# Kernel optimization log

Hardware: AMD Instinct MI355X
Metric: run time of the kernel (lower is better)

The kernel has to match this reference:

```python
import jax, jax.numpy as jnp
import numpy as np

# init kwargs (constants)
MIN_ = 1      # bg samples
MAX_ = 1      # fg samples
KSZ = 3       # dilation kernel size
IGNORE = -255 # seg_ignore_idx
EPS = 1e-6

B, H, W = 128, 512, 512


def setup_inputs() -> dict:
    key = jax.random.key(0)
    k1, k2, k3 = jax.random.split(key, 3)
    x = jax.random.uniform(k1, (B, 1, H, W), dtype=jnp.float32)   # CAM, nonneg
    u_fg = jax.random.uniform(k2, (B, H * W), dtype=jnp.float32)  # noise for fg multinomial
    u_bg = jax.random.uniform(k3, (B, H * W), dtype=jnp.float32)  # noise for bg multinomial
    return {"x": x, "u_fg": u_fg, "u_bg": u_bg}


def _sample_mask(logw, u, k):
    """Weighted sampling without replacement via Gumbel-top-k (== torch.multinomial).
    logw: [B, HW] log-weights; u: [B, HW] uniform noise. Returns binary [B, HW] int32 mask."""
    g = -jnp.log(-jnp.log(jnp.clip(u, 1e-12, 1.0 - 1e-12)))
    idx = jax.lax.top_k(logw + g, k)[1]  # [B, k]
    mask = jnp.zeros(logw.shape, dtype=jnp.int32)
    return mask.at[jnp.arange(logw.shape[0])[:, None], idx].set(1)


def _dilate(m):
    """Morphological dilation of binary mask [B,H,W] with KSZ x KSZ ones structuring element
    == max-pool with SAME padding."""
    if KSZ == 1:
        return m
    return jax.lax.reduce_window(m, jnp.int32(0), jax.lax.max,
                                 (1, KSZ, KSZ), (1, 1, 1), 'SAME')


def reference(x, u_fg, u_bg):
    b, _, h, w = x.shape
    cam = x[:, 0].reshape(b, h * w)
    p = cam + EPS
    p = p / p.sum(axis=1, keepdims=True)           # normalized CAM (fg weights)
    fg = _sample_mask(jnp.log(p), u_fg, MAX_).reshape(b, h, w)
    bg = _sample_mask(jnp.log1p(-p), u_bg, MIN_).reshape(b, h, w)  # bg weights = 1 - p
    fg = _dilate(fg)
    bg = _dilate(bg)
    overlap = (fg + bg) == 2
    fg = jnp.where(overlap, 0, fg)
    bg = jnp.where(overlap, 0, bg)
    out = jnp.full((b, h, w), IGNORE, dtype=jnp.int32)
    out = jnp.where(fg == 1, 1, out)
    out = jnp.where(bg == 1, 0, out)  # bg written last, as in torch
    return out
```

## Files before the change

### kernel.cpp

```cpp
#include <hip/hip_runtime.h>

#define NB 128
#define HH 512
#define WW 512
#define HW (HH * WW)

constexpr float EPS_F = 1e-6f;
constexpr int IGNORE_V = -255;

constexpr int TPB = 256;
constexpr int G = 4;
constexpr int NG = 4;
constexpr int F4T = G * NG;
constexpr int EPB = TPB * F4T * 4;
constexpr int BPR = HW / EPB;

typedef float floatx4 __attribute__((ext_vector_type(4)));
typedef int intx4 __attribute__((ext_vector_type(4)));

__device__ inline unsigned long long pack_key(float f, unsigned idx) {
    unsigned bits = __float_as_uint(f);
    bits ^= (bits & 0x80000000u) ? 0xFFFFFFFFu : 0x80000000u;
    return ((unsigned long long)bits << 32) | (unsigned)(~idx);
}

__global__ __launch_bounds__(TPB, 4) void k_fg_sum_fill(const float* __restrict__ cam,
                                                        const float* __restrict__ ufg,
                                                        int* __restrict__ out,
                                                        float* __restrict__ partial,
                                                        unsigned long long* __restrict__ bestFg) {
    const int b = blockIdx.y, chunk = blockIdx.x, t = threadIdx.x;
    const long base = (long)b * HW + (long)chunk * EPB;
    const floatx4* c4 = (const floatx4*)(cam + base);
    const floatx4* f4 = (const floatx4*)(ufg + base);
    intx4* o4 = (intx4*)(out + base);
    const intx4 fill = {IGNORE_V, IGNORE_V, IGNORE_V, IGNORE_V};

    floatx4 cb[2][G], ub[2][G];
#pragma unroll
    for (int k = 0; k < G; ++k) {
        cb[0][k] = c4[t + k * TPB];
        ub[0][k] = __builtin_nontemporal_load(&f4[t + k * TPB]);
    }

    float s = 0.f;
    unsigned long long bf = 0ull;
#pragma unroll
    for (int g = 0; g < NG; ++g) {
        const int cur = g & 1, nxt = cur ^ 1;
        if (g + 1 < NG) {
#pragma unroll
            for (int k = 0; k < G; ++k) {
                cb[nxt][k] = c4[t + ((g + 1) * G + k) * TPB];
                ub[nxt][k] = __builtin_nontemporal_load(&f4[t + ((g + 1) * G + k) * TPB]);
            }
        }
#pragma unroll
        for (int k = 0; k < G; ++k) {
            const int slot = g * G + k;
            __builtin_nontemporal_store(fill, &o4[t + slot * TPB]);
            floatx4 v = cb[cur][k];
            floatx4 uu = ub[cur][k];
            const unsigned idx0 = (unsigned)chunk * (unsigned)EPB + (unsigned)(t + slot * TPB) * 4u;
#pragma unroll
            for (int j = 0; j < 4; ++j) {
                float a = v[j] + EPS_F;
                s += a;
                float E = -logf(fmaxf(uu[j], 1e-12f));
                unsigned long long kf = pack_key(a / E, idx0 + j);
                bf = kf > bf ? kf : bf;
            }
        }
    }

#pragma unroll
    for (int off = 32; off > 0; off >>= 1) {
        s += __shfl_down(s, off, 64);
        unsigned long long of = __shfl_down(bf, off, 64);
        bf = of > bf ? of : bf;
    }
    __shared__ float ls[TPB / 64];
    __shared__ unsigned long long lf[TPB / 64];
    if ((t & 63) == 0) { ls[t >> 6] = s; lf[t >> 6] = bf; }
    __syncthreads();
    if (t == 0) {
        float tot = 0.f;
#pragma unroll
        for (int w = 0; w < TPB / 64; ++w) {
            tot += ls[w];
            if (lf[w] > bf) bf = lf[w];
        }
        partial[b * BPR + chunk] = tot;
        bestFg[b * BPR + chunk] = bf;
    }
}

__global__ __launch_bounds__(TPB, 4) void k_bg(const float* __restrict__ cam,
                                               const float* __restrict__ ubg,
                                               const float* __restrict__ partial,
                                               unsigned long long* __restrict__ bestBg) {
    const int b = blockIdx.y, chunk = blockIdx.x, t = threadIdx.x;

    float S = 0.f;
    for (int i = 0; i < BPR; ++i) S += partial[b * BPR + i];

    const long base = (long)b * HW + (long)chunk * EPB;
    const floatx4* c4 = (const floatx4*)(cam + base);
    const floatx4* g4 = (const floatx4*)(ubg + base);

    floatx4 cb[2][G], ub[2][G];
#pragma unroll
    for (int k = 0; k < G; ++k) {
        cb[0][k] = __builtin_nontemporal_load(&c4[t + k * TPB]);
        ub[0][k] = __builtin_nontemporal_load(&g4[t + k * TPB]);
    }

    unsigned long long bb = 0ull;
#pragma unroll
    for (int g = 0; g < NG; ++g) {
        const int cur = g & 1, nxt = cur ^ 1;
        if (g + 1 < NG) {
#pragma unroll
            for (int k = 0; k < G; ++k) {
                cb[nxt][k] = __builtin_nontemporal_load(&c4[t + ((g + 1) * G + k) * TPB]);
                ub[nxt][k] = __builtin_nontemporal_load(&g4[t + ((g + 1) * G + k) * TPB]);
            }
        }
#pragma unroll
        for (int k = 0; k < G; ++k) {
            const int slot = g * G + k;
            floatx4 v = cb[cur][k];
            floatx4 uu = ub[cur][k];
            const unsigned idx0 = (unsigned)chunk * (unsigned)EPB + (unsigned)(t + slot * TPB) * 4u;
#pragma unroll
            for (int j = 0; j < 4; ++j) {
                float num = S - (v[j] + EPS_F);
                float E = -logf(fmaxf(uu[j], 1e-12f));
                unsigned long long kb = pack_key(num / E, idx0 + j);
                bb = kb > bb ? kb : bb;
            }
        }
    }

#pragma unroll
    for (int off = 32; off > 0; off >>= 1) {
        unsigned long long ob = __shfl_down(bb, off, 64);
        bb = ob > bb ? ob : bb;
    }
    __shared__ unsigned long long lb[TPB / 64];
    if ((t & 63) == 0) lb[t >> 6] = bb;
    __syncthreads();
    if (t == 0) {
        for (int w = 1; w < TPB / 64; ++w)
            if (lb[w] > bb) bb = lb[w];
        bestBg[b * BPR + chunk] = bb;
    }
}

__global__ void k_fixup(const unsigned long long* __restrict__ bestFg,
                        const unsigned long long* __restrict__ bestBg,
                        int* __restrict__ out) {
    const int b = threadIdx.x;
    if (b >= NB) return;
    unsigned long long bf = 0ull, bb = 0ull;
    for (int i = 0; i < BPR; ++i) {
        unsigned long long f = bestFg[b * BPR + i];
        unsigned long long g = bestBg[b * BPR + i];
        if (f > bf) bf = f;
        if (g > bb) bb = g;
    }
    const unsigned fidx = ~(unsigned)(bf & 0xFFFFFFFFull);
    const unsigned bidx = ~(unsigned)(bb & 0xFFFFFFFFull);
    const int fr = (int)(fidx / WW), fc = (int)(fidx % WW);
    const int br = (int)(bidx / WW), bc = (int)(bidx % WW);
    const long rb = (long)b * HW;

    for (int dr = -1; dr <= 1; ++dr) {
        for (int dc = -1; dc <= 1; ++dc) {
            int r = fr + dr, c = fc + dc;
            if (r >= 0 && r < HH && c >= 0 && c < WW) {
                bool inBg = (r >= br - 1 && r <= br + 1 && c >= bc - 1 && c <= bc + 1);
                if (!inBg) out[rb + (long)r * WW + c] = 1;
            }
            r = br + dr; c = bc + dc;
            if (r >= 0 && r < HH && c >= 0 && c < WW) {
                bool inFg = (r >= fr - 1 && r <= fr + 1 && c >= fc - 1 && c <= fc + 1);
                if (!inFg) out[rb + (long)r * WW + c] = 0;
            }
        }
    }
}

extern "C" void kernel_launch(void* const* d_in, const int* in_sizes, int n_in,
                              void* d_out, int out_size, void* d_ws, size_t ws_size,
                              hipStream_t stream) {
    const float* cam = (const float*)d_in[0];
    const float* ufg = (const float*)d_in[1];
    const float* ubg = (const float*)d_in[2];
    int* out = (int*)d_out;

    float* partial = (float*)d_ws;
    unsigned long long* bestFg = (unsigned long long*)((char*)d_ws + 8192);
    unsigned long long* bestBg = (unsigned long long*)((char*)d_ws + 24576);

    dim3 grid(BPR, NB);
    k_fg_sum_fill<<<grid, TPB, 0, stream>>>(cam, ufg, out, partial, bestFg);
    k_bg<<<grid, TPB, 0, stream>>>(cam, ubg, partial, bestBg);
    k_fixup<<<1, 128, 0, stream>>>(bestFg, bestBg, out);
}
```

Measured before the change: 412.1 us.

## Move fg scoring into second pass alongside bg scoring

The fg Gumbel-max scoring, along with its read of the u_fg noise, moves out of the first kernel, which now only sums the CAM and fills the output. The second kernel reads cam, u_fg and u_bg together and computes both fg and bg keys, using smaller prefetch groups to keep register pressure in check. Total bytes moved stay about the same. The work between the two passes is rebalanced: the first pass becomes a light streaming pass and the second carries both log-heavy computations. The second kernel now holds more registers per thread and issues more loads in flight.

```diff
diff --git a/kernel.cpp b/kernel.cpp
--- a/kernel.cpp
+++ b/kernel.cpp
@@ -15,6 +15,9 @@
 constexpr int EPB = TPB * F4T * 4;
 constexpr int BPR = HW / EPB;
 
+constexpr int G2 = 2;
+constexpr int NG2 = 8;
+
 typedef float floatx4 __attribute__((ext_vector_type(4)));
 typedef int intx4 __attribute__((ext_vector_type(4)));
 
@@ -24,81 +27,59 @@
     return ((unsigned long long)bits << 32) | (unsigned)(~idx);
 }
 
-__global__ __launch_bounds__(TPB, 4) void k_fg_sum_fill(const float* __restrict__ cam,
-                                                        const float* __restrict__ ufg,
-                                                        int* __restrict__ out,
-                                                        float* __restrict__ partial,
-                                                        unsigned long long* __restrict__ bestFg) {
+__global__ __launch_bounds__(TPB, 4) void k_sum_fill(const float* __restrict__ cam,
+                                                     int* __restrict__ out,
+                                                     float* __restrict__ partial) {
     const int b = blockIdx.y, chunk = blockIdx.x, t = threadIdx.x;
     const long base = (long)b * HW + (long)chunk * EPB;
     const floatx4* c4 = (const floatx4*)(cam + base);
-    const floatx4* f4 = (const floatx4*)(ufg + base);
     intx4* o4 = (intx4*)(out + base);
     const intx4 fill = {IGNORE_V, IGNORE_V, IGNORE_V, IGNORE_V};
 
-    floatx4 cb[2][G], ub[2][G];
-#pragma unroll
-    for (int k = 0; k < G; ++k) {
-        cb[0][k] = c4[t + k * TPB];
-        ub[0][k] = __builtin_nontemporal_load(&f4[t + k * TPB]);
-    }
+    floatx4 cb[2][G];
+#pragma unroll
+    for (int k = 0; k < G; ++k) cb[0][k] = c4[t + k * TPB];
 
     float s = 0.f;
-    unsigned long long bf = 0ull;
 #pragma unroll
     for (int g = 0; g < NG; ++g) {
         const int cur = g & 1, nxt = cur ^ 1;
         if (g + 1 < NG) {
 #pragma unroll
-            for (int k = 0; k < G; ++k) {
-                cb[nxt][k] = c4[t + ((g + 1) * G + k) * TPB];
-                ub[nxt][k] = __builtin_nontemporal_load(&f4[t + ((g + 1) * G + k) * TPB]);
-            }
+            for (int k = 0; k < G; ++k) cb[nxt][k] = c4[t + ((g + 1) * G + k) * TPB];
         }
 #pragma unroll
         for (int k = 0; k < G; ++k) {
             const int slot = g * G + k;
             __builtin_nontemporal_store(fill, &o4[t + slot * TPB]);
             floatx4 v = cb[cur][k];
-            floatx4 uu = ub[cur][k];
-            const unsigned idx0 = (unsigned)chunk * (unsigned)EPB + (unsigned)(t + slot * TPB) * 4u;
 #pragma unroll
             for (int j = 0; j < 4; ++j) {
                 float a = v[j] + EPS_F;
                 s += a;
-                float E = -logf(fmaxf(uu[j], 1e-12f));
-                unsigned long long kf = pack_key(a / E, idx0 + j);
-                bf = kf > bf ? kf : bf;
-            }
-        }
-    }
-
-#pragma unroll
-    for (int off = 32; off > 0; off >>= 1) {
-        s += __shfl_down(s, off, 64);
-        unsigned long long of = __shfl_down(bf, off, 64);
-        bf = of > bf ? of : bf;
-    }
+            }
+        }
+    }
+
+#pragma unroll
+    for (int off = 32; off > 0; off >>= 1) s += __shfl_down(s, off, 64);
     __shared__ float ls[TPB / 64];
-    __shared__ unsigned long long lf[TPB / 64];
-    if ((t & 63) == 0) { ls[t >> 6] = s; lf[t >> 6] = bf; }
+    if ((t & 63) == 0) ls[t >> 6] = s;
     __syncthreads();
     if (t == 0) {
         float tot = 0.f;
 #pragma unroll
-        for (int w = 0; w < TPB / 64; ++w) {
-            tot += ls[w];
-            if (lf[w] > bf) bf = lf[w];
-        }
+        for (int w = 0; w < TPB / 64; ++w) tot += ls[w];
         partial[b * BPR + chunk] = tot;
-        bestFg[b * BPR + chunk] = bf;
-    }
-}
-
-__global__ __launch_bounds__(TPB, 4) void k_bg(const float* __restrict__ cam,
-                                               const float* __restrict__ ubg,
-                                               const float* __restrict__ partial,
-                                               unsigned long long* __restrict__ bestBg) {
+    }
+}
+
+__global__ __launch_bounds__(TPB, 4) void k_score(const float* __restrict__ cam,
+                                                  const float* __restrict__ ufg,
+                                                  const float* __restrict__ ubg,
+                                                  const float* __restrict__ partial,
+                                                  unsigned long long* __restrict__ bestFg,
+                                                  unsigned long long* __restrict__ bestBg) {
     const int b = blockIdx.y, chunk = blockIdx.x, t = threadIdx.x;
 
     float S = 0.f;
@@ -106,37 +87,44 @@
 
     const long base = (long)b * HW + (long)chunk * EPB;
     const floatx4* c4 = (const floatx4*)(cam + base);
+    const floatx4* f4 = (const floatx4*)(ufg + base);
     const floatx4* g4 = (const floatx4*)(ubg + base);
 
-    floatx4 cb[2][G], ub[2][G];
-#pragma unroll
-    for (int k = 0; k < G; ++k) {
-        cb[0][k] = __builtin_nontemporal_load(&c4[t + k * TPB]);
-        ub[0][k] = __builtin_nontemporal_load(&g4[t + k * TPB]);
-    }
-
-    unsigned long long bb = 0ull;
-#pragma unroll
-    for (int g = 0; g < NG; ++g) {
+    floatx4 cb[2][G2], fb[2][G2], gb[2][G2];
+#pragma unroll
+    for (int k = 0; k < G2; ++k) {
+        cb[0][k] = c4[t + k * TPB];
+        fb[0][k] = __builtin_nontemporal_load(&f4[t + k * TPB]);
+        gb[0][k] = __builtin_nontemporal_load(&g4[t + k * TPB]);
+    }
+
+    unsigned long long bf = 0ull, bb = 0ull;
+#pragma unroll
+    for (int g = 0; g < NG2; ++g) {
         const int cur = g & 1, nxt = cur ^ 1;
-        if (g + 1 < NG) {
-#pragma unroll
-            for (int k = 0; k < G; ++k) {
-                cb[nxt][k] = __builtin_nontemporal_load(&c4[t + ((g + 1) * G + k) * TPB]);
-                ub[nxt][k] = __builtin_nontemporal_load(&g4[t + ((g + 1) * G + k) * TPB]);
-            }
-        }
-#pragma unroll
-        for (int k = 0; k < G; ++k) {
-            const int slot = g * G + k;
+        if (g + 1 < NG2) {
+#pragma unroll
+            for (int k = 0; k < G2; ++k) {
+                cb[nxt][k] = c4[t + ((g + 1) * G2 + k) * TPB];
+                fb[nxt][k] = __builtin_nontemporal_load(&f4[t + ((g + 1) * G2 + k) * TPB]);
+                gb[nxt][k] = __builtin_nontemporal_load(&g4[t + ((g + 1) * G2 + k) * TPB]);
+            }
+        }
+#pragma unroll
+        for (int k = 0; k < G2; ++k) {
+            const int slot = g * G2 + k;
             floatx4 v = cb[cur][k];
-            floatx4 uu = ub[cur][k];
+            floatx4 uf = fb[cur][k];
+            floatx4 ug = gb[cur][k];
             const unsigned idx0 = (unsigned)chunk * (unsigned)EPB + (unsigned)(t + slot * TPB) * 4u;
 #pragma unroll
             for (int j = 0; j < 4; ++j) {
-                float num = S - (v[j] + EPS_F);
-                float E = -logf(fmaxf(uu[j], 1e-12f));
-                unsigned long long kb = pack_key(num / E, idx0 + j);
+                float a = v[j] + EPS_F;
+                float Ef = -logf(fmaxf(uf[j], 1e-12f));
+                unsigned long long kf = pack_key(a / Ef, idx0 + j);
+                bf = kf > bf ? kf : bf;
+                float Eb = -logf(fmaxf(ug[j], 1e-12f));
+                unsigned long long kb = pack_key((S - a) / Eb, idx0 + j);
                 bb = kb > bb ? kb : bb;
             }
         }
@@ -144,15 +132,22 @@
 
 #pragma unroll
     for (int off = 32; off > 0; off >>= 1) {
+        unsigned long long of = __shfl_down(bf, off, 64);
+        bf = of > bf ? of : bf;
         unsigned long long ob = __shfl_down(bb, off, 64);
         bb = ob > bb ? ob : bb;
     }
+    __shared__ unsigned long long lf[TPB / 64];
     __shared__ unsigned long long lb[TPB / 64];
-    if ((t & 63) == 0) lb[t >> 6] = bb;
+    if ((t & 63) == 0) { lf[t >> 6] = bf; lb[t >> 6] = bb; }
     __syncthreads();
     if (t == 0) {
-        for (int w = 1; w < TPB / 64; ++w)
+#pragma unroll
+        for (int w = 1; w < TPB / 64; ++w) {
+            if (lf[w] > bf) bf = lf[w];
             if (lb[w] > bb) bb = lb[w];
+        }
+        bestFg[b * BPR + chunk] = bf;
         bestBg[b * BPR + chunk] = bb;
     }
 }
@@ -204,7 +199,7 @@
     unsigned long long* bestBg = (unsigned long long*)((char*)d_ws + 24576);
 
     dim3 grid(BPR, NB);
-    k_fg_sum_fill<<<grid, TPB, 0, stream>>>(cam, ufg, out, partial, bestFg);
-    k_bg<<<grid, TPB, 0, stream>>>(cam, ubg, partial, bestBg);
+    k_sum_fill<<<grid, TPB, 0, stream>>>(cam, out, partial);
+    k_score<<<grid, TPB, 0, stream>>>(cam, ufg, ubg, partial, bestFg, bestBg);
     k_fixup<<<1, 128, 0, stream>>>(bestFg, bestBg, out);
 }
```

New measurement: 496.3 us. 20.4% more time.

## Shrink per-block tiles, raise occupancy, and merge per-row maxima with atomics

Applied to the files above, without the earlier changes.

Reduces the elements handled per block from 16K to 4K, quadrupling the grid and raising launch occupancy bounds, and drops the manual double buffering in favour of issuing all loads up front. Per-row best keys are now combined with 64-bit atomicMax into a zero-initialised buffer, so the fixup kernel reads one value per row. Key packing is simplified on the assumption that all keys are positive. In exchange it adds an init kernel launch, more partial sums to reduce in the bg kernel, and atomic contention.

```diff
diff --git a/kernel.cpp b/kernel.cpp
--- a/kernel.cpp
+++ b/kernel.cpp
@@ -9,26 +9,28 @@
 constexpr int IGNORE_V = -255;
 
 constexpr int TPB = 256;
-constexpr int G = 4;
-constexpr int NG = 4;
-constexpr int F4T = G * NG;
-constexpr int EPB = TPB * F4T * 4;
+constexpr int VPT = 4;
+constexpr int EPB = TPB * VPT * 4;
 constexpr int BPR = HW / EPB;
 
 typedef float floatx4 __attribute__((ext_vector_type(4)));
 typedef int intx4 __attribute__((ext_vector_type(4)));
 
-__device__ inline unsigned long long pack_key(float f, unsigned idx) {
-    unsigned bits = __float_as_uint(f);
-    bits ^= (bits & 0x80000000u) ? 0xFFFFFFFFu : 0x80000000u;
+__device__ inline unsigned long long pack_key_pos(float f, unsigned idx) {
+    unsigned bits = __float_as_uint(f) | 0x80000000u;
     return ((unsigned long long)bits << 32) | (unsigned)(~idx);
 }
 
-__global__ __launch_bounds__(TPB, 4) void k_fg_sum_fill(const float* __restrict__ cam,
-                                                        const float* __restrict__ ufg,
-                                                        int* __restrict__ out,
-                                                        float* __restrict__ partial,
-                                                        unsigned long long* __restrict__ bestFg) {
+__global__ void k_init(unsigned long long* __restrict__ best) {
+    const int t = threadIdx.x;
+    if (t < 2 * NB) best[t] = 0ull;
+}
+
+__global__ __launch_bounds__(TPB, 8) void k_fg(const float* __restrict__ cam,
+                                               const float* __restrict__ ufg,
+                                               int* __restrict__ out,
+                                               float* __restrict__ partial,
+                                               unsigned long long* __restrict__ bestFg) {
     const int b = blockIdx.y, chunk = blockIdx.x, t = threadIdx.x;
     const long base = (long)b * HW + (long)chunk * EPB;
     const floatx4* c4 = (const floatx4*)(cam + base);
@@ -36,40 +38,26 @@
     intx4* o4 = (intx4*)(out + base);
     const intx4 fill = {IGNORE_V, IGNORE_V, IGNORE_V, IGNORE_V};
 
-    floatx4 cb[2][G], ub[2][G];
+    floatx4 cv[VPT], uv[VPT];
 #pragma unroll
-    for (int k = 0; k < G; ++k) {
-        cb[0][k] = c4[t + k * TPB];
-        ub[0][k] = __builtin_nontemporal_load(&f4[t + k * TPB]);
-    }
+    for (int k = 0; k < VPT; ++k) cv[k] = c4[t + k * TPB];
+#pragma unroll
+    for (int k = 0; k < VPT; ++k) uv[k] = __builtin_nontemporal_load(&f4[t + k * TPB]);
+#pragma unroll
+    for (int k = 0; k < VPT; ++k) __builtin_nontemporal_store(fill, &o4[t + k * TPB]);
 
     float s = 0.f;
     unsigned long long bf = 0ull;
 #pragma unroll
-    for (int g = 0; g < NG; ++g) {
-        const int cur = g & 1, nxt = cur ^ 1;
-        if (g + 1 < NG) {
+    for (int k = 0; k < VPT; ++k) {
+        const unsigned idx0 = (unsigned)chunk * (unsigned)EPB + (unsigned)(t + k * TPB) * 4u;
 #pragma unroll
-            for (int k = 0; k < G; ++k) {
-                cb[nxt][k] = c4[t + ((g + 1) * G + k) * TPB];
-                ub[nxt][k] = __builtin_nontemporal_load(&f4[t + ((g + 1) * G + k) * TPB]);
-            }
-        }
-#pragma unroll
-        for (int k = 0; k < G; ++k) {
-            const int slot = g * G + k;
-            __builtin_nontemporal_store(fill, &o4[t + slot * TPB]);
-            floatx4 v = cb[cur][k];
-            floatx4 uu = ub[cur][k];
-            const unsigned idx0 = (unsigned)chunk * (unsigned)EPB + (unsigned)(t + slot * TPB) * 4u;
-#pragma unroll
-            for (int j = 0; j < 4; ++j) {
-                float a = v[j] + EPS_F;
-                s += a;
-                float E = -logf(fmaxf(uu[j], 1e-12f));
-                unsigned long long kf = pack_key(a / E, idx0 + j);
-                bf = kf > bf ? kf : bf;
-            }
+        for (int j = 0; j < 4; ++j) {
+            float a = cv[k][j] + EPS_F;
+            s += a;
+            float E = -logf(fmaxf(uv[k][j], 1e-12f));
+            unsigned long long kf = pack_key_pos(a / E, idx0 + j);
+            bf = kf > bf ? kf : bf;
         }
     }
 
@@ -91,54 +79,38 @@
             if (lf[w] > bf) bf = lf[w];
         }
         partial[b * BPR + chunk] = tot;
-        bestFg[b * BPR + chunk] = bf;
+        atomicMax(&bestFg[b], bf);
     }
 }
 
-__global__ __launch_bounds__(TPB, 4) void k_bg(const float* __restrict__ cam,
+__global__ __launch_bounds__(TPB, 8) void k_bg(const float* __restrict__ cam,
                                                const float* __restrict__ ubg,
                                                const float* __restrict__ partial,
                                                unsigned long long* __restrict__ bestBg) {
     const int b = blockIdx.y, chunk = blockIdx.x, t = threadIdx.x;
+    const long base = (long)b * HW + (long)chunk * EPB;
+    const floatx4* c4 = (const floatx4*)(cam + base);
+    const floatx4* g4 = (const floatx4*)(ubg + base);
+
+    floatx4 cv[VPT], uv[VPT];
+#pragma unroll
+    for (int k = 0; k < VPT; ++k) cv[k] = c4[t + k * TPB];
+#pragma unroll
+    for (int k = 0; k < VPT; ++k) uv[k] = __builtin_nontemporal_load(&g4[t + k * TPB]);
 
     float S = 0.f;
     for (int i = 0; i < BPR; ++i) S += partial[b * BPR + i];
 
-    const long base = (long)b * HW + (long)chunk * EPB;
-    const floatx4* c4 = (const floatx4*)(cam + base);
-    const floatx4* g4 = (const floatx4*)(ubg + base);
-
-    floatx4 cb[2][G], ub[2][G];
-#pragma unroll
-    for (int k = 0; k < G; ++k) {
-        cb[0][k] = __builtin_nontemporal_load(&c4[t + k * TPB]);
-        ub[0][k] = __builtin_nontemporal_load(&g4[t + k * TPB]);
-    }
-
     unsigned long long bb = 0ull;
 #pragma unroll
-    for (int g = 0; g < NG; ++g) {
-        const int cur = g & 1, nxt = cur ^ 1;
-        if (g + 1 < NG) {
+    for (int k = 0; k < VPT; ++k) {
+        const unsigned idx0 = (unsigned)chunk * (unsigned)EPB + (unsigned)(t + k * TPB) * 4u;
 #pragma unroll
-            for (int k = 0; k < G; ++k) {
-                cb[nxt][k] = __builtin_nontemporal_load(&c4[t + ((g + 1) * G + k) * TPB]);
-                ub[nxt][k] = __builtin_nontemporal_load(&g4[t + ((g + 1) * G + k) * TPB]);
-            }
-        }
-#pragma unroll
-        for (int k = 0; k < G; ++k) {
-            const int slot = g * G + k;
-            floatx4 v = cb[cur][k];
-            floatx4 uu = ub[cur][k];
-            const unsigned idx0 = (unsigned)chunk * (unsigned)EPB + (unsigned)(t + slot * TPB) * 4u;
-#pragma unroll
-            for (int j = 0; j < 4; ++j) {
-                float num = S - (v[j] + EPS_F);
-                float E = -logf(fmaxf(uu[j], 1e-12f));
-                unsigned long long kb = pack_key(num / E, idx0 + j);
-                bb = kb > bb ? kb : bb;
-            }
+        for (int j = 0; j < 4; ++j) {
+            float num = S - (cv[k][j] + EPS_F);
+            float E = -logf(fmaxf(uv[k][j], 1e-12f));
+            unsigned long long kb = pack_key_pos(num / E, idx0 + j);
+            bb = kb > bb ? kb : bb;
         }
     }
 
@@ -151,9 +123,10 @@
     if ((t & 63) == 0) lb[t >> 6] = bb;
     __syncthreads();
     if (t == 0) {
+#pragma unroll
         for (int w = 1; w < TPB / 64; ++w)
             if (lb[w] > bb) bb = lb[w];
-        bestBg[b * BPR + chunk] = bb;
+        atomicMax(&bestBg[b], bb);
     }
 }
 
@@ -162,13 +135,8 @@
                         int* __restrict__ out) {
     const int b = threadIdx.x;
     if (b >= NB) return;
-    unsigned long long bf = 0ull, bb = 0ull;
-    for (int i = 0; i < BPR; ++i) {
-        unsigned long long f = bestFg[b * BPR + i];
-        unsigned long long g = bestBg[b * BPR + i];
-        if (f > bf) bf = f;
-        if (g > bb) bb = g;
-    }
+    const unsigned long long bf = bestFg[b];
+    const unsigned long long bb = bestBg[b];
     const unsigned fidx = ~(unsigned)(bf & 0xFFFFFFFFull);
     const unsigned bidx = ~(unsigned)(bb & 0xFFFFFFFFull);
     const int fr = (int)(fidx / WW), fc = (int)(fidx % WW);
@@ -200,11 +168,13 @@
     int* out = (int*)d_out;
 
     float* partial = (float*)d_ws;
-    unsigned long long* bestFg = (unsigned long long*)((char*)d_ws + 8192);
-    unsigned long long* bestBg = (unsigned long long*)((char*)d_ws + 24576);
+    unsigned long long* best = (unsigned long long*)((char*)d_ws + 32768);
+    unsigned long long* bestFg = best;
+    unsigned long long* bestBg = best + NB;
 
     dim3 grid(BPR, NB);
-    k_fg_sum_fill<<<grid, TPB, 0, stream>>>(cam, ufg, out, partial, bestFg);
+    k_init<<<1, 256, 0, stream>>>(best);
+    k_fg<<<grid, TPB, 0, stream>>>(cam, ufg, out, partial, bestFg);
     k_bg<<<grid, TPB, 0, stream>>>(cam, ubg, partial, bestBg);
     k_fixup<<<1, 128, 0, stream>>>(bestFg, bestBg, out);
 }
```

Measured after the change: 406.0 us. About the same (-1.5%).
